# Kernel optimization log

Hardware: AMD Instinct MI355X
Metric: run time of the kernel (lower is better)

## Reference

```python
import jax, jax.numpy as jnp
import numpy as np

EPS = 1e-08
SPARSITY = 0.1  # fraction of (node, hyperedge) incidences set to 1


def setup_inputs() -> dict:
    key = jax.random.key(0)
    k_x, k_w, k_h, k_W, k_b = jax.random.split(key, 5)
    B, N, E, Din, Dout = 8, 4096, 2048, 256, 256
    x = jax.random.normal(k_x, (B, N, Din), dtype=jnp.float32)
    edge_weight = jax.random.uniform(k_w, (E,), dtype=jnp.float32)
    H = (jax.random.uniform(k_h, (N, E)) < SPARSITY).astype(jnp.float32)
    # nn.Linear params
    bound = 1.0 / np.sqrt(Din)
    W = jax.random.uniform(k_W, (Dout, Din), minval=-bound, maxval=bound, dtype=jnp.float32)
    b = jax.random.uniform(k_b, (Dout,), minval=-bound, maxval=bound, dtype=jnp.float32)
    return {"x": x, "edge_weight": edge_weight, "H": H, "W": W, "b": b}


def _build_adjacency(H, edge_weight):
    # dv = H @ diag(w) @ 1 = H @ w ; de = H.sum(0)
    dv = H @ edge_weight                      # [N]
    de = H.sum(axis=0)                        # [E]
    dv_is = jnp.power(dv + EPS, -0.5)         # Dv^{-1/2} diagonal
    de_inv = jnp.power(de + EPS, -1.0)        # De^{-1} diagonal
    # A = Dv^{-1/2} H W De^{-1} H^T Dv^{-1/2}; apply diagonals as row/col scales
    Hw = H * (edge_weight * de_inv)[None, :]  # [N, E]
    A = (dv_is[:, None] * (Hw @ H.T)) * dv_is[None, :]  # [N, N]
    return A


def reference(x, edge_weight, H, W, b):
    A = _build_adjacency(H, edge_weight)
    xw = jnp.einsum('bnd,od->bno', x, W) + b  # Linear: [B, N, Dout]
    out = jnp.einsum('ij,bjd->bid', A, xw)    # hypergraph propagation
    return out
```

## Files before the change

kernel.cpp:

```cpp
#include <hip/hip_runtime.h>
#include <hip/hip_bf16.h>

typedef __hip_bfloat16 bf16;
typedef __bf16 bfx8 __attribute__((ext_vector_type(8)));
typedef float f32x4 __attribute__((ext_vector_type(4)));

#define BM 128

typedef __attribute__((address_space(3))) void lds_void_t;
typedef const __attribute__((address_space(1))) void gbl_void_t;

__global__ void prep_kernel(const float* __restrict__ H, const float* __restrict__ w,
                            bf16* __restrict__ HT, bf16* __restrict__ Hb,
                            float* __restrict__ de, float* __restrict__ dvr, int N, int E) {
    __shared__ bf16 tile[64][65];
    __shared__ float cred[4][64];
    __shared__ float rred[4][64];
    int eb = blockIdx.x * 64, nb = blockIdx.y * 64;
    int tid = threadIdx.x;
    int c = tid & 63, g = tid >> 6;

    float cs = 0.f;
#pragma unroll
    for (int k = 0; k < 16; k++) {
        int r = g + (k << 2);
        float v = H[(size_t)(nb + r) * E + eb + c];
        bf16 bv = __float2bfloat16(v);
        tile[r][c] = bv;
        Hb[(size_t)(nb + r) * E + eb + c] = bv;
        cs += v;
    }
    cred[g][c] = cs;
    __syncthreads();
    if (g == 0) {
        float s = cred[0][c] + cred[1][c] + cred[2][c] + cred[3][c];
        atomicAdd(&de[eb + c], s);
    }
    float rs = 0.f;
#pragma unroll
    for (int k = 0; k < 16; k++) {
        int cc = g + (k << 2);
        rs += __bfloat162float(tile[c][cc]) * w[eb + cc];
    }
    rred[g][c] = rs;
    __syncthreads();
    if (g == 1) {
        float s = rred[0][c] + rred[1][c] + rred[2][c] + rred[3][c];
        atomicAdd(&dvr[nb + c], s);
    }
#pragma unroll
    for (int k = 0; k < 16; k++) {
        int r = g + (k << 2);
        HT[(size_t)(eb + r) * N + nb + c] = tile[c][r];
    }
}

__global__ void finalize_kernel(const float* __restrict__ dvr, const float* __restrict__ de,
                                const float* __restrict__ w, float* __restrict__ dv_is,
                                float* __restrict__ wsc, int N, int E) {
    int i = blockIdx.x * 256 + threadIdx.x;
    if (i < N) dv_is[i] = rsqrtf(dvr[i] + 1e-8f);
    if (i < E) wsc[i] = w[i] / (de[i] + 1e-8f);
}

template <int MODE, int RY>
__global__ __launch_bounds__(256) void gemm_bt_async(
    const bf16* __restrict__ A, const bf16* __restrict__ Bt, int K,
    void* __restrict__ Cv, int ldc,
    const float* __restrict__ rvec, const float* __restrict__ cvec) {
    __shared__ __align__(16) bf16 SA[2][BM * 32];
    __shared__ __align__(16) bf16 SB[2][64 * 32];

    const int lin = blockIdx.y * gridDim.x + blockIdx.x;
    const int xcd = lin & 7, sidx = lin >> 3;
    const int bx = (xcd & 3) * 8 + (sidx & 7);
    const int by = (xcd >> 2) * RY + (sidx >> 3);

    const int tid     = threadIdx.x;
    const int rowBase = by * BM;
    const int colBase = bx * 64;
    const int wave = tid >> 6, lane = tid & 63;
    const int wr = (wave >> 1) * 64;
    const int wc = (wave & 1) * 32;
    const int lcol = lane & 15, quad = lane >> 4;

    const int sr = tid >> 2, skc = (tid & 3) << 3;
    const bf16* a0 = &A[(size_t)(rowBase + sr) * K + skc];
    const bf16* a1 = a0 + (size_t)64 * K;
    const bf16* b0 = &Bt[(size_t)(colBase + sr) * K + skc];
    bf16* d_a0[2] = {&SA[0][sr * 32 + skc], &SA[1][sr * 32 + skc]};
    bf16* d_a1[2] = {&SA[0][(sr + 64) * 32 + skc], &SA[1][(sr + 64) * 32 + skc]};
    bf16* d_b0[2] = {&SB[0][sr * 32 + skc], &SB[1][sr * 32 + skc]};

    f32x4 acc[4][2];
#pragma unroll
    for (int i = 0; i < 4; i++)
#pragma unroll
        for (int j = 0; j < 2; j++) acc[i][j] = (f32x4){0.f, 0.f, 0.f, 0.f};

    for (int k0 = 0; k0 < K; k0 += 64) {
#pragma unroll
        for (int h = 0; h < 2; h++) {
            int kk = k0 + h * 32;
            __builtin_amdgcn_global_load_lds((gbl_void_t*)(a0 + kk), (lds_void_t*)d_a0[h], 16, 0, 0);
            __builtin_amdgcn_global_load_lds((gbl_void_t*)(a1 + kk), (lds_void_t*)d_a1[h], 16, 0, 0);
            __builtin_amdgcn_global_load_lds((gbl_void_t*)(b0 + kk), (lds_void_t*)d_b0[h], 16, 0, 0);
        }
        __syncthreads();

#pragma unroll
        for (int h = 0; h < 2; h++) {
            bfx8 af[4], bfr[2];
#pragma unroll
            for (int i = 0; i < 4; i++)
                af[i] = *(const bfx8*)&SA[h][(wr + i * 16 + lcol) * 32 + quad * 8];
#pragma unroll
            for (int j = 0; j < 2; j++)
                bfr[j] = *(const bfx8*)&SB[h][(wc + j * 16 + lcol) * 32 + quad * 8];
#pragma unroll
            for (int i = 0; i < 4; i++)
#pragma unroll
                for (int j = 0; j < 2; j++)
                    acc[i][j] = __builtin_amdgcn_mfma_f32_16x16x32_bf16(af[i], bfr[j], acc[i][j], 0, 0, 0);
        }
        __syncthreads();
    }

    bf16*  Cb = (bf16*)Cv;
    float* Cf = (float*)Cv;
#pragma unroll
    for (int i = 0; i < 4; i++) {
#pragma unroll
        for (int j = 0; j < 2; j++) {
#pragma unroll
            for (int r = 0; r < 4; r++) {
                int grow = rowBase + wr + i * 16 + quad * 4 + r;
                int gcol = colBase + wc + j * 16 + lcol;
                float v = acc[i][j][r];
                if (MODE == 1) {
                    Cb[(size_t)grow * ldc + gcol] = __float2bfloat16(v * cvec[gcol]);
                } else {
                    Cf[(size_t)(gcol >> 8) * 1048576 + (size_t)grow * 256 + (gcol & 255)] =
                        v * rvec[grow];
                }
            }
        }
    }
}

__global__ __launch_bounds__(256) void gemm_bt_conv(
    const float* __restrict__ A, const float* __restrict__ B, int K,
    bf16* __restrict__ C, int ldc,
    const float* __restrict__ rvec, const float* __restrict__ cvec,
    long long bStride, long long cStride) {
    __shared__ __align__(16) bf16 As[BM * 40];
    __shared__ __align__(16) bf16 Bs[BM * 40];

    const float* Bp = B + (size_t)blockIdx.z * (size_t)bStride;
    bf16*        Cp = C + (size_t)blockIdx.z * (size_t)cStride;

    const int tid     = threadIdx.x;
    const int rowBase = blockIdx.y * BM;
    const int colBase = blockIdx.x * BM;
    const int wave = tid >> 6, lane = tid & 63;
    const int wr = (wave >> 1) * 64;
    const int wc = (wave & 1) * 64;
    const int lcol = lane & 15, quad = lane >> 4;

    f32x4 acc[4][4];
#pragma unroll
    for (int i = 0; i < 4; i++)
#pragma unroll
        for (int j = 0; j < 4; j++) acc[i][j] = (f32x4){0.f, 0.f, 0.f, 0.f};

    for (int k0 = 0; k0 < K; k0 += 32) {
#pragma unroll
        for (int c = 0; c < 2; c++) {
            int ch = tid + c * 256;
            int r = ch >> 2, kc = (ch & 3) << 3;
            size_t aoff = (size_t)(rowBase + r) * K + k0 + kc;
            size_t boff = (size_t)(colBase + r) * K + k0 + kc;
            f32x4 p0 = *(const f32x4*)&A[aoff];
            f32x4 p1 = *(const f32x4*)&A[aoff + 4];
            bfx8 va;
#pragma unroll
            for (int t = 0; t < 4; t++) { va[t] = (__bf16)p0[t]; va[4 + t] = (__bf16)p1[t]; }
            *(bfx8*)&As[r * 40 + kc] = va;
            f32x4 q0 = *(const f32x4*)&Bp[boff];
            f32x4 q1 = *(const f32x4*)&Bp[boff + 4];
            bfx8 vb;
#pragma unroll
            for (int t = 0; t < 4; t++) { vb[t] = (__bf16)q0[t]; vb[4 + t] = (__bf16)q1[t]; }
            *(bfx8*)&Bs[r * 40 + kc] = vb;
        }
        __syncthreads();

        bfx8 af[4], bfr[4];
#pragma unroll
        for (int i = 0; i < 4; i++)
            af[i] = *(const bfx8*)&As[(wr + i * 16 + lcol) * 40 + quad * 8];
#pragma unroll
        for (int j = 0; j < 4; j++)
            bfr[j] = *(const bfx8*)&Bs[(wc + j * 16 + lcol) * 40 + quad * 8];
#pragma unroll
        for (int i = 0; i < 4; i++)
#pragma unroll
            for (int j = 0; j < 4; j++)
                acc[i][j] = __builtin_amdgcn_mfma_f32_16x16x32_bf16(af[i], bfr[j], acc[i][j], 0, 0, 0);
        __syncthreads();
    }

#pragma unroll
    for (int i = 0; i < 4; i++) {
#pragma unroll
        for (int j = 0; j < 4; j++) {
#pragma unroll
            for (int r = 0; r < 4; r++) {
                int grow = rowBase + wr + i * 16 + quad * 4 + r;
                int gcol = colBase + wc + j * 16 + lcol;
                float v = (acc[i][j][r] + rvec[grow]) * cvec[gcol];
                Cp[(size_t)grow * ldc + gcol] = __float2bfloat16(v);
            }
        }
    }
}

extern "C" void kernel_launch(void* const* d_in, const int* in_sizes, int n_in,
                              void* d_out, int out_size, void* d_ws, size_t ws_size,
                              hipStream_t stream) {
    const float* x    = (const float*)d_in[0];
    const float* ew   = (const float*)d_in[1];
    const float* H    = (const float*)d_in[2];
    const float* W    = (const float*)d_in[3];
    const float* bias = (const float*)d_in[4];
    float* out = (float*)d_out;

    const int N = 4096, E = 2048;

    char* ws = (char*)d_ws;
    float* de    = (float*)(ws);
    float* dvr   = (float*)(ws + 8192);
    float* dv_is = (float*)(ws + 24576);
    float* wsc   = (float*)(ws + 40960);
    bf16*  HT    = (bf16*)(ws + 65536);
    bf16*  xs_t  = (bf16*)(ws + 65536 + 16777216);
    bf16*  t_t   = (bf16*)(ws + 65536 + 2 * 16777216);

    bf16* Hb = (bf16*)d_out;

    hipMemsetAsync(ws, 0, 24576, stream);

    prep_kernel<<<dim3(E / 64, N / 64), 256, 0, stream>>>(H, ew, HT, Hb, de, dvr, N, E);
    finalize_kernel<<<dim3(16), 256, 0, stream>>>(dvr, de, ew, dv_is, wsc, N, E);

    gemm_bt_conv<<<dim3(4096 / BM, 256 / BM, 8), 256, 0, stream>>>(
        W, x, 256, xs_t, 4096, bias, dv_is, 1048576LL, 1048576LL);

    gemm_bt_async<1, 8><<<dim3(32, 16), 256, 0, stream>>>(
        xs_t, HT, 4096, t_t, 2048, nullptr, wsc);

    hipMemcpyAsync(xs_t, Hb, 16777216, hipMemcpyDeviceToDevice, stream);

    gemm_bt_async<2, 16><<<dim3(32, 32), 256, 0, stream>>>(
        (const bf16*)xs_t, t_t, 2048, out, 0, dv_is, nullptr);
}
```

Measured before the change: 241.0 us.

## Split-K the first bf16 GEMM into two slices with a combine kernel

The xs·H GEMM, with K=4096, now runs over a z-dimension of two K-halves, doubling the number of workgroups. Each half writes its bf16 partial result to scratch space in the unused upper half of the output buffer. A new elementwise kernel adds the two partials and applies the per-edge weight scaling. The aim is more in-flight blocks per CU to hide memory latency on the long K loop. The cost is extra global traffic for the partials, one more launch, and an extra bf16 rounding of the partial sums.

```diff
diff --git a/kernel.cpp b/kernel.cpp
--- a/kernel.cpp
+++ b/kernel.cpp
@@ -63,9 +63,22 @@
     if (i < E) wsc[i] = w[i] / (de[i] + 1e-8f);
 }
 
+__global__ void combine_kernel(const bf16* __restrict__ s0, const bf16* __restrict__ s1,
+                               const float* __restrict__ wsc, bf16* __restrict__ tt) {
+    size_t i = ((size_t)blockIdx.x * 256 + threadIdx.x) * 8;
+    size_t e = i & 2047;
+    bfx8 a = *(const bfx8*)&s0[i];
+    bfx8 b = *(const bfx8*)&s1[i];
+    bfx8 v;
+#pragma unroll
+    for (int t = 0; t < 8; t++)
+        v[t] = (__bf16)(((float)a[t] + (float)b[t]) * wsc[e + t]);
+    *(bfx8*)&tt[i] = v;
+}
+
 template <int MODE, int RY>
 __global__ __launch_bounds__(256) void gemm_bt_async(
-    const bf16* __restrict__ A, const bf16* __restrict__ Bt, int K,
+    const bf16* __restrict__ A, const bf16* __restrict__ Bt, int Kst, int kLen,
     void* __restrict__ Cv, int ldc,
     const float* __restrict__ rvec, const float* __restrict__ cvec) {
     __shared__ __align__(16) bf16 SA[2][BM * 32];
@@ -75,6 +88,8 @@
     const int xcd = lin & 7, sidx = lin >> 3;
     const int bx = (xcd & 3) * 8 + (sidx & 7);
     const int by = (xcd >> 2) * RY + (sidx >> 3);
+
+    const int kBase = (MODE == 3) ? blockIdx.z * kLen : 0;
 
     const int tid     = threadIdx.x;
     const int rowBase = by * BM;
@@ -85,9 +100,9 @@
     const int lcol = lane & 15, quad = lane >> 4;
 
     const int sr = tid >> 2, skc = (tid & 3) << 3;
-    const bf16* a0 = &A[(size_t)(rowBase + sr) * K + skc];
-    const bf16* a1 = a0 + (size_t)64 * K;
-    const bf16* b0 = &Bt[(size_t)(colBase + sr) * K + skc];
+    const bf16* a0 = &A[(size_t)(rowBase + sr) * Kst + kBase + skc];
+    const bf16* a1 = a0 + (size_t)64 * Kst;
+    const bf16* b0 = &Bt[(size_t)(colBase + sr) * Kst + kBase + skc];
     bf16* d_a0[2] = {&SA[0][sr * 32 + skc], &SA[1][sr * 32 + skc]};
     bf16* d_a1[2] = {&SA[0][(sr + 64) * 32 + skc], &SA[1][(sr + 64) * 32 + skc]};
     bf16* d_b0[2] = {&SB[0][sr * 32 + skc], &SB[1][sr * 32 + skc]};
@@ -98,7 +113,7 @@
 #pragma unroll
         for (int j = 0; j < 2; j++) acc[i][j] = (f32x4){0.f, 0.f, 0.f, 0.f};
 
-    for (int k0 = 0; k0 < K; k0 += 64) {
+    for (int k0 = 0; k0 < kLen; k0 += 64) {
 #pragma unroll
         for (int h = 0; h < 2; h++) {
             int kk = k0 + h * 32;
@@ -128,6 +143,7 @@
 
     bf16*  Cb = (bf16*)Cv;
     float* Cf = (float*)Cv;
+    const size_t sliceOff = (MODE == 3) ? (size_t)blockIdx.z * 4194304 : 0;
 #pragma unroll
     for (int i = 0; i < 4; i++) {
 #pragma unroll
@@ -137,8 +153,8 @@
                 int grow = rowBase + wr + i * 16 + quad * 4 + r;
                 int gcol = colBase + wc + j * 16 + lcol;
                 float v = acc[i][j][r];
-                if (MODE == 1) {
-                    Cb[(size_t)grow * ldc + gcol] = __float2bfloat16(v * cvec[gcol]);
+                if (MODE == 3) {
+                    Cb[sliceOff + (size_t)grow * ldc + gcol] = __float2bfloat16(v);
                 } else {
                     Cf[(size_t)(gcol >> 8) * 1048576 + (size_t)grow * 256 + (gcol & 255)] =
                         v * rvec[grow];
@@ -246,7 +262,8 @@
     bf16*  xs_t  = (bf16*)(ws + 65536 + 16777216);
     bf16*  t_t   = (bf16*)(ws + 65536 + 2 * 16777216);
 
-    bf16* Hb = (bf16*)d_out;
+    bf16* Hb     = (bf16*)d_out;
+    bf16* slices = (bf16*)((char*)d_out + 16777216);
 
     hipMemsetAsync(ws, 0, 24576, stream);
 
@@ -256,11 +273,14 @@
     gemm_bt_conv<<<dim3(4096 / BM, 256 / BM, 8), 256, 0, stream>>>(
         W, x, 256, xs_t, 4096, bias, dv_is, 1048576LL, 1048576LL);
 
-    gemm_bt_async<1, 8><<<dim3(32, 16), 256, 0, stream>>>(
-        xs_t, HT, 4096, t_t, 2048, nullptr, wsc);
+    gemm_bt_async<3, 8><<<dim3(32, 16, 2), 256, 0, stream>>>(
+        xs_t, HT, 4096, 2048, slices, 2048, nullptr, nullptr);
+
+    combine_kernel<<<dim3(2048), 256, 0, stream>>>(
+        slices, slices + 4194304, wsc, t_t);
 
     hipMemcpyAsync(xs_t, Hb, 16777216, hipMemcpyDeviceToDevice, stream);
 
     gemm_bt_async<2, 16><<<dim3(32, 32), 256, 0, stream>>>(
-        (const bf16*)xs_t, t_t, 2048, out, 0, dv_is, nullptr);
-}
+        (const bf16*)xs_t, t_t, 2048, 2048, out, 0, dv_is, nullptr);
+}
```

Result: faster. 234.3 us (-2.8%).

## Split-K the H^T GEMM, pre-convert inputs to bf16, fuse combine with copy

Applied to the files above, without the earlier changes.

Replaces the fp32-loading linear GEMM with a bf16 conversion pass followed by the async-LDS GEMM (MODE 0, batched over z). The 4096-K propagation GEMM is split three ways along K across grid z, writing partial bf16 results that a new combine kernel sums and scales by wsc, fused with the Hb copy that replaces hipMemcpyAsync. The aim is more parallelism for the previously 512-block GEMM and a cheaper linear GEMM. The cost is extra kernel launches, extra memory traffic for the partial sums, and rounding each partial to bf16.

```diff
diff --git a/kernel.cpp b/kernel.cpp
--- a/kernel.cpp
+++ b/kernel.cpp
@@ -63,18 +63,69 @@
     if (i < E) wsc[i] = w[i] / (de[i] + 1e-8f);
 }
 
+__global__ void conv_kernel(const float* __restrict__ x, const float* __restrict__ W,
+                            bf16* __restrict__ xb, bf16* __restrict__ Wb) {
+    int bid = blockIdx.x;
+    const float* src = (bid < 4096) ? x : W;
+    bf16*        dst = (bid < 4096) ? xb : Wb;
+    size_t base = (bid < 4096) ? (size_t)bid : (size_t)(bid - 4096);
+    size_t i = (base * 256 + threadIdx.x) * 8;
+    f32x4 p0 = *(const f32x4*)&src[i];
+    f32x4 p1 = *(const f32x4*)&src[i + 4];
+    bfx8 v;
+#pragma unroll
+    for (int t = 0; t < 4; t++) { v[t] = (__bf16)p0[t]; v[4 + t] = (__bf16)p1[t]; }
+    *(bfx8*)&dst[i] = v;
+}
+
+__global__ void combine_copy_kernel(const bf16* __restrict__ s0, const bf16* __restrict__ s1,
+                                    const bf16* s2, const float* __restrict__ wsc,
+                                    bf16* tt,
+                                    const bf16* __restrict__ Hb, bf16* __restrict__ HbC) {
+    int bid = blockIdx.x;
+    if (bid < 2048) {
+        size_t i = ((size_t)bid * 256 + threadIdx.x) * 8;
+        size_t e = i & 2047;
+        bfx8 a = *(const bfx8*)&s0[i];
+        bfx8 b = *(const bfx8*)&s1[i];
+        bfx8 c = *(const bfx8*)&s2[i];
+        bfx8 v;
+#pragma unroll
+        for (int t = 0; t < 8; t++)
+            v[t] = (__bf16)(((float)a[t] + (float)b[t] + (float)c[t]) * wsc[e + t]);
+        *(bfx8*)&tt[i] = v;
+    } else {
+        size_t j = (((size_t)(bid - 2048)) * 256 + threadIdx.x) * 16;
+        bfx8 u0 = *(const bfx8*)&Hb[j];
+        bfx8 u1 = *(const bfx8*)&Hb[j + 8];
+        *(bfx8*)&HbC[j] = u0;
+        *(bfx8*)&HbC[j + 8] = u1;
+    }
+}
+
 template <int MODE, int RY>
 __global__ __launch_bounds__(256) void gemm_bt_async(
-    const bf16* __restrict__ A, const bf16* __restrict__ Bt, int K,
-    void* __restrict__ Cv, int ldc,
+    const bf16* __restrict__ A, const bf16* __restrict__ Bt, int Kst,
+    void* __restrict__ Cv, void* __restrict__ Cv2, int ldc,
     const float* __restrict__ rvec, const float* __restrict__ cvec) {
     __shared__ __align__(16) bf16 SA[2][BM * 32];
     __shared__ __align__(16) bf16 SB[2][64 * 32];
 
-    const int lin = blockIdx.y * gridDim.x + blockIdx.x;
-    const int xcd = lin & 7, sidx = lin >> 3;
-    const int bx = (xcd & 3) * 8 + (sidx & 7);
-    const int by = (xcd >> 2) * RY + (sidx >> 3);
+    int bx, by;
+    if (MODE == 0) {
+        bx = blockIdx.x; by = blockIdx.y;
+    } else {
+        const int lin = blockIdx.y * 32 + blockIdx.x;
+        const int xcd = lin & 7, sidx = lin >> 3;
+        bx = (xcd & 3) * 8 + (sidx & 7);
+        by = (xcd >> 2) * RY + (sidx >> 3);
+    }
+
+    int kBase = 0, kLen = Kst;
+    if (MODE == 2) kLen = 2048;
+    if (MODE == 3) { kBase = blockIdx.z * 1344; kLen = (blockIdx.z == 2) ? 1408 : 1344; }
+
+    const bf16* Bp = (MODE == 0) ? Bt + (size_t)blockIdx.z * 1048576 : Bt;
 
     const int tid     = threadIdx.x;
     const int rowBase = by * BM;
@@ -85,9 +136,9 @@
     const int lcol = lane & 15, quad = lane >> 4;
 
     const int sr = tid >> 2, skc = (tid & 3) << 3;
-    const bf16* a0 = &A[(size_t)(rowBase + sr) * K + skc];
-    const bf16* a1 = a0 + (size_t)64 * K;
-    const bf16* b0 = &Bt[(size_t)(colBase + sr) * K + skc];
+    const bf16* a0 = &A[(size_t)(rowBase + sr) * Kst + kBase + skc];
+    const bf16* a1 = a0 + (size_t)64 * Kst;
+    const bf16* b0 = &Bp[(size_t)(colBase + sr) * Kst + kBase + skc];
     bf16* d_a0[2] = {&SA[0][sr * 32 + skc], &SA[1][sr * 32 + skc]};
     bf16* d_a1[2] = {&SA[0][(sr + 64) * 32 + skc], &SA[1][(sr + 64) * 32 + skc]};
     bf16* d_b0[2] = {&SB[0][sr * 32 + skc], &SB[1][sr * 32 + skc]};
@@ -98,7 +149,7 @@
 #pragma unroll
         for (int j = 0; j < 2; j++) acc[i][j] = (f32x4){0.f, 0.f, 0.f, 0.f};
 
-    for (int k0 = 0; k0 < K; k0 += 64) {
+    for (int k0 = 0; k0 < kLen; k0 += 64) {
 #pragma unroll
         for (int h = 0; h < 2; h++) {
             int kk = k0 + h * 32;
@@ -126,8 +177,11 @@
         __syncthreads();
     }
 
-    bf16*  Cb = (bf16*)Cv;
+    bf16* Cb = (bf16*)Cv;
+    if (MODE == 3 && blockIdx.z == 2) Cb = (bf16*)Cv2;
+    if (MODE == 3 && blockIdx.z == 1) Cb = (bf16*)Cv + 4194304;
     float* Cf = (float*)Cv;
+    const size_t cRowOff = (MODE == 0) ? (size_t)blockIdx.z * 256 : 0;
 #pragma unroll
     for (int i = 0; i < 4; i++) {
 #pragma unroll
@@ -137,89 +191,15 @@
                 int grow = rowBase + wr + i * 16 + quad * 4 + r;
                 int gcol = colBase + wc + j * 16 + lcol;
                 float v = acc[i][j][r];
-                if (MODE == 1) {
-                    Cb[(size_t)grow * ldc + gcol] = __float2bfloat16(v * cvec[gcol]);
+                if (MODE == 0) {
+                    v = (v + rvec[grow]) * cvec[gcol];
+                    Cb[(cRowOff + grow) * (size_t)ldc + gcol] = __float2bfloat16(v);
+                } else if (MODE == 3) {
+                    Cb[(size_t)grow * ldc + gcol] = __float2bfloat16(v);
                 } else {
                     Cf[(size_t)(gcol >> 8) * 1048576 + (size_t)grow * 256 + (gcol & 255)] =
                         v * rvec[grow];
                 }
-            }
-        }
-    }
-}
-
-__global__ __launch_bounds__(256) void gemm_bt_conv(
-    const float* __restrict__ A, const float* __restrict__ B, int K,
-    bf16* __restrict__ C, int ldc,
-    const float* __restrict__ rvec, const float* __restrict__ cvec,
-    long long bStride, long long cStride) {
-    __shared__ __align__(16) bf16 As[BM * 40];
-    __shared__ __align__(16) bf16 Bs[BM * 40];
-
-    const float* Bp = B + (size_t)blockIdx.z * (size_t)bStride;
-    bf16*        Cp = C + (size_t)blockIdx.z * (size_t)cStride;
-
-    const int tid     = threadIdx.x;
-    const int rowBase = blockIdx.y * BM;
-    const int colBase = blockIdx.x * BM;
-    const int wave = tid >> 6, lane = tid & 63;
-    const int wr = (wave >> 1) * 64;
-    const int wc = (wave & 1) * 64;
-    const int lcol = lane & 15, quad = lane >> 4;
-
-    f32x4 acc[4][4];
-#pragma unroll
-    for (int i = 0; i < 4; i++)
-#pragma unroll
-        for (int j = 0; j < 4; j++) acc[i][j] = (f32x4){0.f, 0.f, 0.f, 0.f};
-
-    for (int k0 = 0; k0 < K; k0 += 32) {
-#pragma unroll
-        for (int c = 0; c < 2; c++) {
-            int ch = tid + c * 256;
-            int r = ch >> 2, kc = (ch & 3) << 3;
-            size_t aoff = (size_t)(rowBase + r) * K + k0 + kc;
-            size_t boff = (size_t)(colBase + r) * K + k0 + kc;
-            f32x4 p0 = *(const f32x4*)&A[aoff];
-            f32x4 p1 = *(const f32x4*)&A[aoff + 4];
-            bfx8 va;
-#pragma unroll
-            for (int t = 0; t < 4; t++) { va[t] = (__bf16)p0[t]; va[4 + t] = (__bf16)p1[t]; }
-            *(bfx8*)&As[r * 40 + kc] = va;
-            f32x4 q0 = *(const f32x4*)&Bp[boff];
-            f32x4 q1 = *(const f32x4*)&Bp[boff + 4];
-            bfx8 vb;
-#pragma unroll
-            for (int t = 0; t < 4; t++) { vb[t] = (__bf16)q0[t]; vb[4 + t] = (__bf16)q1[t]; }
-            *(bfx8*)&Bs[r * 40 + kc] = vb;
-        }
-        __syncthreads();
-
-        bfx8 af[4], bfr[4];
-#pragma unroll
-        for (int i = 0; i < 4; i++)
-            af[i] = *(const bfx8*)&As[(wr + i * 16 + lcol) * 40 + quad * 8];
-#pragma unroll
-        for (int j = 0; j < 4; j++)
-            bfr[j] = *(const bfx8*)&Bs[(wc + j * 16 + lcol) * 40 + quad * 8];
-#pragma unroll
-        for (int i = 0; i < 4; i++)
-#pragma unroll
-            for (int j = 0; j < 4; j++)
-                acc[i][j] = __builtin_amdgcn_mfma_f32_16x16x32_bf16(af[i], bfr[j], acc[i][j], 0, 0, 0);
-        __syncthreads();
-    }
-
-#pragma unroll
-    for (int i = 0; i < 4; i++) {
-#pragma unroll
-        for (int j = 0; j < 4; j++) {
-#pragma unroll
-            for (int r = 0; r < 4; r++) {
-                int grow = rowBase + wr + i * 16 + quad * 4 + r;
-                int gcol = colBase + wc + j * 16 + lcol;
-                float v = (acc[i][j][r] + rvec[grow]) * cvec[gcol];
-                Cp[(size_t)grow * ldc + gcol] = __float2bfloat16(v);
             }
         }
     }
@@ -243,24 +223,29 @@
     float* dv_is = (float*)(ws + 24576);
     float* wsc   = (float*)(ws + 40960);
     bf16*  HT    = (bf16*)(ws + 65536);
-    bf16*  xs_t  = (bf16*)(ws + 65536 + 16777216);
-    bf16*  t_t   = (bf16*)(ws + 65536 + 2 * 16777216);
+    bf16*  slot2 = (bf16*)(ws + 65536 + 16777216);
+    bf16*  slot3 = (bf16*)(ws + 65536 + 2 * 16777216);
 
     bf16* Hb = (bf16*)d_out;
+    bf16* xb = (bf16*)d_out + 8388608;
+    bf16* s01 = xb;
 
     hipMemsetAsync(ws, 0, 24576, stream);
 
     prep_kernel<<<dim3(E / 64, N / 64), 256, 0, stream>>>(H, ew, HT, Hb, de, dvr, N, E);
     finalize_kernel<<<dim3(16), 256, 0, stream>>>(dvr, de, ew, dv_is, wsc, N, E);
 
-    gemm_bt_conv<<<dim3(4096 / BM, 256 / BM, 8), 256, 0, stream>>>(
-        W, x, 256, xs_t, 4096, bias, dv_is, 1048576LL, 1048576LL);
-
-    gemm_bt_async<1, 8><<<dim3(32, 16), 256, 0, stream>>>(
-        xs_t, HT, 4096, t_t, 2048, nullptr, wsc);
-
-    hipMemcpyAsync(xs_t, Hb, 16777216, hipMemcpyDeviceToDevice, stream);
+    conv_kernel<<<dim3(4128), 256, 0, stream>>>(x, W, xb, slot3);
+
+    gemm_bt_async<0, 0><<<dim3(64, 2, 8), 256, 0, stream>>>(
+        slot3, xb, 256, slot2, nullptr, 4096, bias, dv_is);
+
+    gemm_bt_async<3, 8><<<dim3(32, 16, 3), 256, 0, stream>>>(
+        slot2, HT, 4096, s01, slot3, 2048, nullptr, nullptr);
+
+    combine_copy_kernel<<<dim3(4096), 256, 0, stream>>>(
+        s01, s01 + 4194304, slot3, wsc, slot3, Hb, slot2);
 
     gemm_bt_async<2, 16><<<dim3(32, 32), 256, 0, stream>>>(
-        (const bf16*)xs_t, t_t, 2048, out, 0, dv_is, nullptr);
-}
+        slot2, slot3, 2048, out, nullptr, 0, dv_is, nullptr);
+}
```

New measurement: 238.9 us. About the same (-0.9%).
